# Kernel optimization log

Hardware: AMD Instinct MI355X
Metric: run time of the kernel (lower is better)

## Reference

```python
import jax, jax.numpy as jnp
import numpy as np

N, E, F_IN, F, D, L, G = 50000, 800000, 92, 128, 50, 3, 256
EPS = 1e-5


def _bn(v, g, b):
    # BatchNorm1d in training mode: biased batch stats over axis 0
    mu = jnp.mean(v, axis=0)
    var = jnp.var(v, axis=0)
    return (v - mu) * jax.lax.rsqrt(var + EPS) * g + b


def setup_inputs() -> dict:
    key = jax.random.key(0)
    ks = jax.random.split(key, 16)
    s = lambda *shape: 1.0 / np.sqrt(shape[0])
    inp = {
        "x": jax.random.normal(ks[0], (N, F_IN), dtype=jnp.float32),
        "edge_attr": jax.random.uniform(ks[1], (E, D), dtype=jnp.float32),
        # embedding MLP (2 layers, no bias)
        "w_emb0": jax.random.normal(ks[2], (F_IN, F), dtype=jnp.float32) * s(F_IN),
        "w_emb1": jax.random.normal(ks[3], (F, F), dtype=jnp.float32) * s(F),
        # CGConv params stacked over L layers; z dim = 2F + D
        "wf": jax.random.normal(ks[4], (L, 2 * F + D, F), dtype=jnp.float32) * s(2 * F + D),
        "bf": jnp.zeros((L, F), dtype=jnp.float32),
        "ws": jax.random.normal(ks[5], (L, 2 * F + D, F), dtype=jnp.float32) * s(2 * F + D),
        "bs": jnp.zeros((L, F), dtype=jnp.float32),
        "bn_g": jnp.ones((L, F), dtype=jnp.float32),
        "bn_b": jnp.zeros((L, F), dtype=jnp.float32),
        # head
        "w1": jax.random.normal(ks[6], (F, F), dtype=jnp.float32) * s(F),
        "b1": jnp.zeros((F,), dtype=jnp.float32),
        "bng": jnp.ones((F,), dtype=jnp.float32),
        "bnb": jnp.zeros((F,), dtype=jnp.float32),
        "w2": jax.random.normal(ks[7], (F, 1), dtype=jnp.float32) * s(F),
        "b2": jnp.zeros((1,), dtype=jnp.float32),
        "edge_index": jax.random.randint(ks[8], (2, E), 0, N, dtype=jnp.int64),
        "batch": jnp.sort(jax.random.randint(ks[9], (N,), 0, G, dtype=jnp.int64)),
        "num_graphs": G,
    }
    return inp


def reference(x, edge_attr, w_emb0, w_emb1, wf, bf, ws, bs, bn_g, bn_b,
              w1, b1, bng, bnb, w2, b2, edge_index, batch, num_graphs):
    src, dst = edge_index[0], edge_index[1]  # x_j = x[src], x_i = x[dst]

    # MLP embedding (bias-free), relu between layers, none after last
    h = jax.nn.relu(x @ w_emb0) @ w_emb1  # [N, F]

    gf = jnp.zeros((num_graphs, F), dtype=h.dtype)
    for l in range(L):
        z = jnp.concatenate([h[dst], h[src], edge_attr], axis=-1)  # [E, 2F+D]
        msg = jax.nn.sigmoid(z @ wf[l] + bf[l]) * jax.nn.softplus(z @ ws[l] + bs[l])
        agg = jax.ops.segment_sum(msg, dst, num_segments=N)  # scatter-add
        h = jax.nn.relu(h + _bn(agg, bn_g[l], bn_b[l]))
        gf = gf + jax.ops.segment_max(h, batch, num_segments=num_graphs)

    out = jax.nn.relu(_bn(gf @ w1 + b1, bng, bnb))
    # dropout: identity (eval mode)
    out = out @ w2 + b2  # [G, 1]
    return out.squeeze(-1)
```

## Files before the change

kernel.cpp:

```cpp
#include <hip/hip_runtime.h>
#include <hip/hip_bf16.h>

#define N_NODES 50000
#define N_EDGES 800000
#define FIN 92
#define FD 128
#define DE 50
#define NL 3
#define NG 256
#define MPAD 130
#define NW 4

typedef short short8 __attribute__((ext_vector_type(8)));
typedef float f32x4 __attribute__((ext_vector_type(4)));

__device__ __forceinline__ unsigned short f2bf(float f) {
    unsigned u = __builtin_bit_cast(unsigned, f);
    unsigned r = (u + 0x7FFFu + ((u >> 16) & 1u)) >> 16;
    return (unsigned short)r;
}
__device__ __forceinline__ float bf2f(unsigned short b) {
    unsigned u = ((unsigned)b) << 16;
    return __builtin_bit_cast(float, u);
}
__device__ __forceinline__ unsigned pack2(float a, float b) {
    return (unsigned)f2bf(a) | ((unsigned)f2bf(b) << 16);
}

__device__ __forceinline__ int posFeat(int p) {
    return ((p >> 2) & 7) * 16 + ((p >> 5) << 2) + (p & 3);
}
__device__ __forceinline__ int posFeat2(int p) {
    int q = ((p >> 5) << 3) | (p & 7);
    return ((q >> 2) << 4) + (((p >> 3) & 3) << 2) + (q & 3);
}

template<int K, int NT, int RELU, int BIAS, int OUTMODE>
__global__ __launch_bounds__(256) void gemm_bbg_kernel(
    const unsigned short* __restrict__ Abf, const unsigned short* __restrict__ Bt,
    const float* __restrict__ bias, void* __restrict__ Cout, void* __restrict__ Cout2, int M)
{
    __shared__ short Alds[64][K + 8];
    __shared__ short Blds[64][K + 8];
    const int tid = threadIdx.x;
    const int m0 = blockIdx.x * 64;
    constexpr int SEG = K / 8;
    constexpr int Nc = NT * 64;

    for (int i = tid; i < 64 * SEG; i += 256) {
        int r = i / SEG, sg = i - r * SEG;
        int row = m0 + r;
        short8 va = (row < M) ? *(const short8*)&Abf[(size_t)row * K + sg * 8] : (short8)0;
        *(short8*)&Alds[r][sg * 8] = va;
    }

    const int wv = tid >> 6, lane = tid & 63;
    const int lr = lane & 15, lk = (lane >> 4) * 8;

    for (int nt = 0; nt < NT; ++nt) {
        __syncthreads();
        for (int i = tid; i < 64 * SEG; i += 256) {
            int r = i / SEG, sg = i - r * SEG;
            *(short8*)&Blds[r][sg * 8] = *(const short8*)&Bt[(size_t)(nt * 64 + r) * K + sg * 8];
        }
        __syncthreads();

        f32x4 acc[4];
#pragma unroll
        for (int i = 0; i < 4; ++i) acc[i] = (f32x4)0.f;
#pragma unroll
        for (int k0 = 0; k0 < K; k0 += 32) {
            short8 a = *(const short8*)&Alds[wv * 16 + lr][k0 + lk];
#pragma unroll
            for (int nf = 0; nf < 4; ++nf) {
                short8 b = *(const short8*)&Blds[nf * 16 + lr][k0 + lk];
                acc[nf] = __builtin_amdgcn_mfma_f32_16x16x32_bf16(a, b, acc[nf], 0, 0, 0);
            }
        }
#pragma unroll
        for (int nf = 0; nf < 4; ++nf) {
#pragma unroll
            for (int r = 0; r < 4; ++r) {
                int row = m0 + wv * 16 + (lane >> 4) * 4 + r;
                int col = nt * 64 + nf * 16 + lr;
                if (row < M) {
                    float v = acc[nf][r];
                    if (BIAS) v += bias[col];
                    if (RELU) v = fmaxf(v, 0.f);
                    if (OUTMODE == 1) {
                        ((unsigned short*)Cout)[(size_t)row * Nc + col] = f2bf(v);
                    } else {
                        ((float*)Cout)[(size_t)row * Nc + col] = v;
                        ((unsigned short*)Cout2)[(size_t)row * Nc + col] = f2bf(v);
                    }
                }
            }
        }
    }
}

__global__ __launch_bounds__(256) void x2bf_kernel(
    const float* __restrict__ x, unsigned short* __restrict__ xbf)
{
    int i = blockIdx.x * 256 + threadIdx.x;
    if (i >= N_NODES * 96) return;
    int row = i / 96, k = i - row * 96;
    float v = (k < FIN) ? __builtin_nontemporal_load(&x[(size_t)row * FIN + k]) : 0.f;
    xbf[i] = f2bf(v);
}

__global__ __launch_bounds__(256) void build_wemb_kernel(
    const float* __restrict__ w_emb0, const float* __restrict__ w_emb1,
    unsigned short* __restrict__ w0T, unsigned short* __restrict__ w1T)
{
    int i = blockIdx.x * 256 + threadIdx.x;
    if (i < 128 * 96) {
        int n = i / 96, k = i - n * 96;
        w0T[i] = (k < FIN) ? f2bf(w_emb0[(size_t)k * FD + n]) : 0;
    }
    if (i < 128 * 128) {
        int n = i >> 7, k = i & 127;
        w1T[i] = f2bf(w_emb1[(size_t)k * FD + n]);
    }
}

__global__ __launch_bounds__(256) void build_bcatT_kernel(
    const float* __restrict__ wf, const float* __restrict__ wsw,
    const float* __restrict__ bfb, const float* __restrict__ bsb,
    unsigned short* __restrict__ BcatT, float* __restrict__ bcatF)
{
    int i = blockIdx.x * 256 + threadIdx.x;
    if (i < NL * 512 * 128) {
        int l = i / (512 * 128);
        int r = i - l * 512 * 128;
        int n = r >> 7, k = r & 127;
        int seg = n >> 7, p = n & 127;
        int nf_ = seg * 128 + posFeat2(p);
        const float* Wm = (nf_ < 256) ? wf : wsw;
        int jj = nf_ & 255;
        int krow = (jj < 128) ? k : (128 + k);
        int col = jj & 127;
        BcatT[i] = f2bf(Wm[((size_t)l * 306 + krow) * FD + col]);
    }
    if (i < NL * 512) {
        int l = i >> 9, n = i & 511;
        int seg = n >> 7, p = n & 127;
        float v = 0.f;
        if (seg == 0) v = bfb[l * FD + posFeat2(p)];
        else if (seg == 2) v = bsb[l * FD + posFeat2(p)];
        bcatF[i] = v;
    }
}

__global__ __launch_bounds__(256) void build_wecat_kernel(
    const float* __restrict__ wf, const float* __restrict__ wsw,
    unsigned short* __restrict__ WecatT)
{
    int i = blockIdx.x * 256 + threadIdx.x;
    if (i >= NL * 256 * 64) return;
    int l = i / (256 * 64);
    int r = i - l * 256 * 64;
    int col = r >> 6, k = r & 63;
    float v = 0.f;
    if (k < DE) {
        const float* W = (col < 128) ? wf : wsw;
        v = W[((size_t)l * 306 + 256 + k) * FD + (col & 127)];
    }
    WecatT[i] = f2bf(v);
}

__global__ __launch_bounds__(256) void hist_kernel(
    const int* __restrict__ dstIdx, int* __restrict__ counts)
{
    int e = blockIdx.x * 256 + threadIdx.x;
    if (e < N_EDGES) atomicAdd(&counts[dstIdx[e]], 1);
}

__global__ __launch_bounds__(1024) void scan_kernel(
    const int* __restrict__ counts, int* __restrict__ cursor)
{
    __shared__ int part[1024];
    const int t = threadIdx.x;
    const int CH = 49;
    const int base = t * CH;
    int s = 0;
    for (int i = 0; i < CH; ++i) {
        int idx = base + i;
        if (idx < N_NODES) s += counts[idx];
    }
    part[t] = s;
    __syncthreads();
    int v = s;
    for (int off = 1; off < 1024; off <<= 1) {
        int add = (t >= off) ? part[t - off] : 0;
        __syncthreads();
        v += add;
        part[t] = v;
        __syncthreads();
    }
    int pre = (t == 0) ? 0 : part[t - 1];
    for (int i = 0; i < CH; ++i) {
        int idx = base + i;
        if (idx < N_NODES) {
            cursor[idx] = pre;
            pre += counts[idx];
        }
    }
}

__global__ __launch_bounds__(256) void scatter_kernel(
    const int* __restrict__ eidx, int* __restrict__ cursor,
    int* __restrict__ perm, int* __restrict__ srcS, int* __restrict__ dstS)
{
    int e = blockIdx.x * 256 + threadIdx.x;
    if (e >= N_EDGES) return;
    int d = eidx[N_EDGES + e];
    int pos = atomicAdd(&cursor[d], 1);
    perm[pos] = e;
    srcS[pos] = eidx[e];
    dstS[pos] = d;
}

__global__ __launch_bounds__(256) void ea2bf2_kernel(
    const float* __restrict__ ea, const int* __restrict__ perm,
    unsigned* __restrict__ out)
{
    int t = blockIdx.x * 256 + threadIdx.x;
    if (t >= N_EDGES * 32) return;
    int e = t >> 5, j = t & 31;
    unsigned v = 0;
    if (j < 25) {
        int pe = perm[e];
        unsigned long long u = __builtin_nontemporal_load(
            (const unsigned long long*)(ea + (size_t)pe * DE) + j);
        float lo = __builtin_bit_cast(float, (unsigned)u);
        float hi = __builtin_bit_cast(float, (unsigned)(u >> 32));
        v = pack2(lo, hi);
    }
    out[(size_t)e * 32 + j] = v;
}

__global__ __launch_bounds__(128) void msg13_kernel(
    const unsigned short* __restrict__ Pbf,
    const unsigned short* __restrict__ eabf,
    const unsigned short* __restrict__ WecatT,
    const int* __restrict__ srcS, const int* __restrict__ dstS,
    float* __restrict__ agg)
{
    __shared__ float mlds[32][MPAD];
    __shared__ int dlds[NW * 32 + 2];
    const int tid = threadIdx.x;
    const int base = blockIdx.x * (NW * 32);

    for (int i = tid; i < NW * 32 + 2; i += 128) {
        int ge = base - 1 + i;
        int v;
        if (ge < 0) v = -1;
        else if (ge >= N_EDGES) v = -2;
        else v = __builtin_nontemporal_load(&dstS[ge]);
        dlds[i] = v;
    }

    const int w = tid >> 6, lane = tid & 63;
    const int lr = lane & 15, hi = lane >> 4;
    const int eloc = w * 16 + lr;

    int s_cur = __builtin_nontemporal_load(&srcS[base + eloc]);
    short8 b0_cur = __builtin_nontemporal_load((const short8*)&eabf[(size_t)(base + eloc) * 64 + hi * 8]);
    short8 b1_cur = __builtin_nontemporal_load((const short8*)&eabf[(size_t)(base + eloc) * 64 + 32 + hi * 8]);

    __syncthreads();

    float run = 0.f;
    bool startsInside = (dlds[1] != dlds[0]);
    const int fcol = posFeat(tid);

#pragma unroll 1
    for (int wi = 0; wi < NW; ++wi) {
        const int d = dlds[1 + wi * 32 + eloc];
        const int s = s_cur;
        const short8 b0 = b0_cur, b1 = b1_cur;

        if (wi + 1 < NW) {
            const int en = base + (wi + 1) * 32 + eloc;
            s_cur = __builtin_nontemporal_load(&srcS[en]);
            b0_cur = __builtin_nontemporal_load((const short8*)&eabf[(size_t)en * 64 + hi * 8]);
            b1_cur = __builtin_nontemporal_load((const short8*)&eabf[(size_t)en * 64 + 32 + hi * 8]);
        }

        const unsigned short* pdrow = Pbf + (size_t)d * 512 + hi * 8;
        const unsigned short* psrow = Pbf + (size_t)s * 512 + hi * 8;

        unsigned pvp[16];
        {
            short8 pds[4], pss[4];
#pragma unroll
            for (int i = 0; i < 4; ++i) {
                pds[i] = *(const short8*)(pdrow + 256 + i * 32);
                pss[i] = *(const short8*)(psrow + 384 + i * 32);
            }
            f32x4 accS[8];
#pragma unroll
            for (int i = 0; i < 8; ++i) accS[i] = (f32x4)0.f;
#pragma unroll
            for (int nf = 0; nf < 8; ++nf) {
                short8 a0 = *(const short8*)&WecatT[(size_t)((nf + 8) * 16 + lr) * 64 + hi * 8];
                short8 a1 = *(const short8*)&WecatT[(size_t)((nf + 8) * 16 + lr) * 64 + 32 + hi * 8];
                accS[nf] = __builtin_amdgcn_mfma_f32_16x16x32_bf16(a0, b0, accS[nf], 0, 0, 0);
                accS[nf] = __builtin_amdgcn_mfma_f32_16x16x32_bf16(a1, b1, accS[nf], 0, 0, 0);
            }
#pragma unroll
            for (int j = 0; j < 16; ++j) {
                const int k0 = 2 * j, k1 = 2 * j + 1;
                float v0 = accS[k0 >> 2][k0 & 3] + bf2f((unsigned short)pds[k0 >> 3][k0 & 7])
                                                 + bf2f((unsigned short)pss[k0 >> 3][k0 & 7]);
                float v1 = accS[k1 >> 2][k1 & 3] + bf2f((unsigned short)pds[k1 >> 3][k1 & 7])
                                                 + bf2f((unsigned short)pss[k1 >> 3][k1 & 7]);
                pvp[j] = pack2(v0, v1);
            }
        }

        __syncthreads();

        {
            short8 pdf[4], psf[4];
#pragma unroll
            for (int i = 0; i < 4; ++i) {
                pdf[i] = *(const short8*)(pdrow + i * 32);
                psf[i] = *(const short8*)(psrow + 128 + i * 32);
            }
            f32x4 accF[8];
#pragma unroll
            for (int i = 0; i < 8; ++i) accF[i] = (f32x4)0.f;
#pragma unroll
            for (int nf = 0; nf < 8; ++nf) {
                short8 a0 = *(const short8*)&WecatT[(size_t)(nf * 16 + lr) * 64 + hi * 8];
                short8 a1 = *(const short8*)&WecatT[(size_t)(nf * 16 + lr) * 64 + 32 + hi * 8];
                accF[nf] = __builtin_amdgcn_mfma_f32_16x16x32_bf16(a0, b0, accF[nf], 0, 0, 0);
                accF[nf] = __builtin_amdgcn_mfma_f32_16x16x32_bf16(a1, b1, accF[nf], 0, 0, 0);
            }
#pragma unroll
            for (int nf = 0; nf < 8; ++nf) {
                f32x4 m;
#pragma unroll
                for (int r = 0; r < 4; ++r) {
                    const int q = nf * 4 + r;
                    float pf = accF[nf][r] + bf2f((unsigned short)pdf[q >> 3][q & 7])
                                           + bf2f((unsigned short)psf[q >> 3][q & 7]);
                    unsigned pw = pvp[q >> 1];
                    float pv = (q & 1) ? __builtin_bit_cast(float, pw & 0xFFFF0000u)
                                       : bf2f((unsigned short)(pw & 0xFFFFu));
                    float sig = 1.f / (1.f + __expf(-pf));
                    float tt = __expf(-fabsf(pv));
                    float sp = fmaxf(pv, 0.f) + __logf(1.f + tt);
                    m[r] = sig * sp;
                }
                *(f32x4*)&mlds[eloc][hi * 32 + nf * 4] = m;
            }
        }
        __syncthreads();

        {
            const int c = tid;
#pragma unroll 4
            for (int ee = 0; ee < 32; ++ee) {
                run += mlds[ee][c];
                const int j = wi * 32 + ee;
                int de = dlds[j + 1];
                int dnext = dlds[j + 2];
                if (de != dnext) {
                    if (startsInside) agg[(size_t)de * FD + fcol] = run;
                    else unsafeAtomicAdd(&agg[(size_t)de * FD + fcol], run);
                    run = 0.f;
                    startsInside = true;
                }
            }
        }
    }
    if (run != 0.f)
        unsafeAtomicAdd(&agg[(size_t)dlds[NW * 32] * FD + fcol], run);
}

__global__ __launch_bounds__(256) void bn_stats_kernel(
    const float* __restrict__ agg, float* __restrict__ stats)
{
    __shared__ float sl[256], sql[256];
    const int tid = threadIdx.x;
    const int f = tid & 127;
    float s = 0.f, sq = 0.f;
    for (int row = blockIdx.x * 2 + (tid >> 7); row < N_NODES; row += gridDim.x * 2) {
        float v = agg[(size_t)row * FD + f];
        s += v; sq += v * v;
    }
    sl[tid] = s; sql[tid] = sq;
    __syncthreads();
    if (tid < 128) {
        unsafeAtomicAdd(&stats[f], sl[tid] + sl[tid + 128]);
        unsafeAtomicAdd(&stats[128 + f], sql[tid] + sql[tid + 128]);
    }
}

__global__ __launch_bounds__(256) void bn_update_kernel(
    float* __restrict__ h, unsigned short* __restrict__ hbf,
    const float* __restrict__ agg,
    const float* __restrict__ stats, const float* __restrict__ g,
    const float* __restrict__ b, const int* __restrict__ batch,
    float* __restrict__ gmax)
{
    const int tid = threadIdx.x;
    const int row = blockIdx.x * 2 + (tid >> 7);
    if (row >= N_NODES) return;
    const int f = tid & 127;
    const float inv = 1.f / (float)N_NODES;
    float mu = stats[f] * inv;
    float var = stats[128 + f] * inv - mu * mu;
    float rs = rsqrtf(var + 1e-5f);
    size_t idx = (size_t)row * FD + f;
    float v = h[idx] + (agg[idx] - mu) * rs * g[f] + b[f];
    v = fmaxf(v, 0.f);
    h[idx] = v;
    hbf[idx] = f2bf(v);
    atomicMax((unsigned*)&gmax[batch[row] * FD + f], __float_as_uint(v));
}

__global__ __launch_bounds__(256) void bn_gmax_kernel(
    const float* __restrict__ h, const float* __restrict__ agg,
    const float* __restrict__ stats, const float* __restrict__ g,
    const float* __restrict__ b, const int* __restrict__ batch,
    float* __restrict__ gmax)
{
    const int tid = threadIdx.x;
    const int row = blockIdx.x * 2 + (tid >> 7);
    if (row >= N_NODES) return;
    const int f = tid & 127;
    const float inv = 1.f / (float)N_NODES;
    float mu = stats[f] * inv;
    float var = stats[128 + f] * inv - mu * mu;
    float rs = rsqrtf(var + 1e-5f);
    size_t idx = (size_t)row * FD + f;
    float v = h[idx] + (agg[idx] - mu) * rs * g[f] + b[f];
    v = fmaxf(v, 0.f);
    atomicMax((unsigned*)&gmax[batch[row] * FD + f], __float_as_uint(v));
}

__global__ __launch_bounds__(256) void gf_acc_kernel(float* __restrict__ gf, const float* __restrict__ gmax)
{
    int i = blockIdx.x * 256 + threadIdx.x;
    gf[i] += gmax[i];
}

__global__ __launch_bounds__(128) void head_y_kernel(
    const float* __restrict__ gf, const float* __restrict__ w1,
    const float* __restrict__ b1, float* __restrict__ y)
{
    __shared__ float row[128];
    int g = blockIdx.x, j = threadIdx.x;
    row[j] = gf[g * FD + j];
    __syncthreads();
    float acc = b1[j];
    for (int k = 0; k < FD; ++k) acc = fmaf(row[k], w1[k * FD + j], acc);
    y[g * FD + j] = acc;
}

__global__ __launch_bounds__(128) void head_stats_kernel(
    const float* __restrict__ y, float* __restrict__ hstat)
{
    int f = threadIdx.x;
    float s = 0.f, sq = 0.f;
    for (int g = 0; g < NG; ++g) { float v = y[g * FD + f]; s += v; sq += v * v; }
    float mu = s / (float)NG;
    float var = sq / (float)NG - mu * mu;
    hstat[f] = mu;
    hstat[128 + f] = rsqrtf(var + 1e-5f);
}

__global__ __launch_bounds__(128) void head_out_kernel(
    const float* __restrict__ y, const float* __restrict__ hstat,
    const float* __restrict__ bng, const float* __restrict__ bnb,
    const float* __restrict__ w2, const float* __restrict__ b2,
    float* __restrict__ out)
{
    __shared__ float part[2];
    int g = blockIdx.x, f = threadIdx.x;
    float v = (y[g * FD + f] - hstat[f]) * hstat[128 + f] * bng[f] + bnb[f];
    v = fmaxf(v, 0.f) * w2[f];
    for (int o = 32; o > 0; o >>= 1) v += __shfl_down(v, o);
    if ((f & 63) == 0) part[f >> 6] = v;
    __syncthreads();
    if (f == 0) out[g] = part[0] + part[1] + b2[0];
}

extern "C" void kernel_launch(void* const* d_in, const int* in_sizes, int n_in,
                              void* d_out, int out_size, void* d_ws, size_t ws_size,
                              hipStream_t stream)
{
    const float* x        = (const float*)d_in[0];
    const float* edge_attr= (const float*)d_in[1];
    const float* w_emb0   = (const float*)d_in[2];
    const float* w_emb1   = (const float*)d_in[3];
    const float* wf       = (const float*)d_in[4];
    const float* bf       = (const float*)d_in[5];
    const float* wsw      = (const float*)d_in[6];
    const float* bs       = (const float*)d_in[7];
    const float* bn_g     = (const float*)d_in[8];
    const float* bn_b     = (const float*)d_in[9];
    const float* w1       = (const float*)d_in[10];
    const float* b1       = (const float*)d_in[11];
    const float* bng      = (const float*)d_in[12];
    const float* bnb      = (const float*)d_in[13];
    const float* w2       = (const float*)d_in[14];
    const float* b2       = (const float*)d_in[15];
    const int*   eidx     = (const int*)d_in[16];
    const int*   batch    = (const int*)d_in[17];

    char* base = (char*)d_ws;
    size_t off = 0;
    auto alloc = [&](size_t bytes) -> void* {
        void* p = base + off;
        off += (bytes + 255) & ~(size_t)255;
        return p;
    };
    float*          h      = (float*)alloc((size_t)N_NODES * FD * 4);
    unsigned short* hbf    = (unsigned short*)alloc((size_t)N_NODES * FD * 2);
    unsigned short* Pbf    = (unsigned short*)alloc((size_t)N_NODES * 512 * 2);
    float*          agg    = (float*)alloc((size_t)N_NODES * FD * 4);
    float*          stats  = (float*)alloc(256 * 4);
    float*          gmax   = (float*)alloc((size_t)NG * FD * 4);
    unsigned short* BcatT  = (unsigned short*)alloc((size_t)NL * 512 * 128 * 2);
    unsigned short* WecatT = (unsigned short*)alloc((size_t)NL * 256 * 64 * 2);
    float*          bcatF  = (float*)alloc((size_t)NL * 512 * 4);
    unsigned short* eabf   = (unsigned short*)alloc((size_t)N_EDGES * 64 * 2);
    int*            srcS   = (int*)alloc((size_t)N_EDGES * 4);
    int*            dstS   = (int*)alloc((size_t)N_EDGES * 4);
    unsigned short* xbf    = (unsigned short*)alloc((size_t)N_NODES * 96 * 2);
    unsigned short* w0T    = (unsigned short*)alloc((size_t)128 * 96 * 2);
    unsigned short* w1T    = (unsigned short*)alloc((size_t)128 * 128 * 2);
    float*          gf     = (float*)alloc((size_t)NG * FD * 4);
    float*          y      = (float*)alloc((size_t)NG * FD * 4);
    float*          hstat  = (float*)alloc(256 * 4);

    const size_t msetBytes = (size_t)((char*)gmax + (size_t)NG * FD * 4 - (char*)agg);

    int* perm   = (int*)agg;
    int* counts = perm + N_EDGES;
    int* cursor = counts + N_NODES;
    unsigned short* t0bf = (unsigned short*)agg;

    const int MB = (N_NODES + 63) / 64;

    hipMemsetAsync(counts, 0, (size_t)N_NODES * 4, stream);
    hist_kernel<<<(N_EDGES + 255) / 256, 256, 0, stream>>>(eidx + N_EDGES, counts);
    scan_kernel<<<1, 1024, 0, stream>>>(counts, cursor);
    scatter_kernel<<<(N_EDGES + 255) / 256, 256, 0, stream>>>(eidx, cursor, perm, srcS, dstS);
    ea2bf2_kernel<<<(N_EDGES * 32) / 256, 256, 0, stream>>>(edge_attr, perm, (unsigned*)eabf);

    build_bcatT_kernel<<<(NL * 512 * 128 + 255) / 256, 256, 0, stream>>>(wf, wsw, bf, bs, BcatT, bcatF);
    build_wecat_kernel<<<(NL * 256 * 64 + 255) / 256, 256, 0, stream>>>(wf, wsw, WecatT);
    build_wemb_kernel<<<64, 256, 0, stream>>>(w_emb0, w_emb1, w0T, w1T);
    x2bf_kernel<<<(N_NODES * 96 + 255) / 256, 256, 0, stream>>>(x, xbf);

    gemm_bbg_kernel<96, 2, 1, 0, 1><<<MB, 256, 0, stream>>>(xbf, w0T, nullptr, t0bf, nullptr, N_NODES);
    gemm_bbg_kernel<128, 2, 0, 0, 2><<<MB, 256, 0, stream>>>(t0bf, w1T, nullptr, h, hbf, N_NODES);

    hipMemsetAsync(gf, 0, (size_t)NG * FD * 4, stream);

    for (int l = 0; l < NL; ++l) {
        hipMemsetAsync(agg, 0, msetBytes, stream);

        gemm_bbg_kernel<128, 8, 0, 1, 1><<<MB, 256, 0, stream>>>(
            hbf, BcatT + (size_t)l * 512 * 128, bcatF + (size_t)l * 512, Pbf, nullptr, N_NODES);

        msg13_kernel<<<N_EDGES / (NW * 32), 128, 0, stream>>>(
            Pbf, eabf, WecatT + (size_t)l * 256 * 64, srcS, dstS, agg);

        bn_stats_kernel<<<256, 256, 0, stream>>>(agg, stats);
        if (l < NL - 1) {
            bn_update_kernel<<<(N_NODES + 1) / 2, 256, 0, stream>>>(
                h, hbf, agg, stats, bn_g + l * FD, bn_b + l * FD, batch, gmax);
        } else {
            bn_gmax_kernel<<<(N_NODES + 1) / 2, 256, 0, stream>>>(
                h, agg, stats, bn_g + l * FD, bn_b + l * FD, batch, gmax);
        }
        gf_acc_kernel<<<(NG * FD) / 256, 256, 0, stream>>>(gf, gmax);
    }

    head_y_kernel<<<NG, 128, 0, stream>>>(gf, w1, b1, y);
    head_stats_kernel<<<1, 128, 0, stream>>>(y, hstat);
    head_out_kernel<<<NG, 128, 0, stream>>>(y, hstat, bng, bnb, w2, b2, (float*)d_out);
}
```

Baseline: 1.349 ms.

## Double-buffer GEMM B tiles and msg LDS, keep A in registers, hoist gathers

The node GEMM now holds its A fragments in registers instead of LDS and double-buffers the B tiles, loading the next tile while the current one is consumed. This removes one barrier per N-tile. The message kernel double-buffers its message LDS tile, which lets it drop the barrier between the two MFMA phases, and issues all four gathered P-row loads up front to overlap gather latency. In exchange, register pressure rises in both kernels and LDS use in the message kernel doubles, which may lower occupancy.

```diff
diff --git a/kernel.cpp b/kernel.cpp
--- a/kernel.cpp
+++ b/kernel.cpp
@@ -40,41 +40,48 @@
     const unsigned short* __restrict__ Abf, const unsigned short* __restrict__ Bt,
     const float* __restrict__ bias, void* __restrict__ Cout, void* __restrict__ Cout2, int M)
 {
-    __shared__ short Alds[64][K + 8];
-    __shared__ short Blds[64][K + 8];
+    __shared__ short Blds[2][64][K + 8];
     const int tid = threadIdx.x;
     const int m0 = blockIdx.x * 64;
     constexpr int SEG = K / 8;
     constexpr int Nc = NT * 64;
+    const int wv = tid >> 6, lane = tid & 63;
+    const int lr = lane & 15, lk = (lane >> 4) * 8;
+
+    short8 afr[K / 32];
+    {
+        int arow = m0 + wv * 16 + lr;
+        bool ok = arow < M;
+#pragma unroll
+        for (int i = 0; i < K / 32; ++i)
+            afr[i] = ok ? *(const short8*)&Abf[(size_t)arow * K + i * 32 + lk] : (short8)0;
+    }
 
     for (int i = tid; i < 64 * SEG; i += 256) {
         int r = i / SEG, sg = i - r * SEG;
-        int row = m0 + r;
-        short8 va = (row < M) ? *(const short8*)&Abf[(size_t)row * K + sg * 8] : (short8)0;
-        *(short8*)&Alds[r][sg * 8] = va;
-    }
-
-    const int wv = tid >> 6, lane = tid & 63;
-    const int lr = lane & 15, lk = (lane >> 4) * 8;
+        *(short8*)&Blds[0][r][sg * 8] = *(const short8*)&Bt[(size_t)r * K + sg * 8];
+    }
+    __syncthreads();
 
     for (int nt = 0; nt < NT; ++nt) {
-        __syncthreads();
-        for (int i = tid; i < 64 * SEG; i += 256) {
-            int r = i / SEG, sg = i - r * SEG;
-            *(short8*)&Blds[r][sg * 8] = *(const short8*)&Bt[(size_t)(nt * 64 + r) * K + sg * 8];
-        }
-        __syncthreads();
+        const int cur = nt & 1;
+        if (nt + 1 < NT) {
+            for (int i = tid; i < 64 * SEG; i += 256) {
+                int r = i / SEG, sg = i - r * SEG;
+                *(short8*)&Blds[cur ^ 1][r][sg * 8] =
+                    *(const short8*)&Bt[(size_t)((nt + 1) * 64 + r) * K + sg * 8];
+            }
+        }
 
         f32x4 acc[4];
 #pragma unroll
         for (int i = 0; i < 4; ++i) acc[i] = (f32x4)0.f;
 #pragma unroll
-        for (int k0 = 0; k0 < K; k0 += 32) {
-            short8 a = *(const short8*)&Alds[wv * 16 + lr][k0 + lk];
+        for (int k0 = 0; k0 < K / 32; ++k0) {
 #pragma unroll
             for (int nf = 0; nf < 4; ++nf) {
-                short8 b = *(const short8*)&Blds[nf * 16 + lr][k0 + lk];
-                acc[nf] = __builtin_amdgcn_mfma_f32_16x16x32_bf16(a, b, acc[nf], 0, 0, 0);
+                short8 b = *(const short8*)&Blds[cur][nf * 16 + lr][k0 * 32 + lk];
+                acc[nf] = __builtin_amdgcn_mfma_f32_16x16x32_bf16(afr[k0], b, acc[nf], 0, 0, 0);
             }
         }
 #pragma unroll
@@ -96,6 +103,7 @@
                 }
             }
         }
+        __syncthreads();
     }
 }
 
@@ -240,14 +248,14 @@
     out[(size_t)e * 32 + j] = v;
 }
 
-__global__ __launch_bounds__(128) void msg13_kernel(
+__global__ __launch_bounds__(128) void msg14_kernel(
     const unsigned short* __restrict__ Pbf,
     const unsigned short* __restrict__ eabf,
     const unsigned short* __restrict__ WecatT,
     const int* __restrict__ srcS, const int* __restrict__ dstS,
     float* __restrict__ agg)
 {
-    __shared__ float mlds[32][MPAD];
+    __shared__ float mlds[2][32][MPAD];
     __shared__ int dlds[NW * 32 + 2];
     const int tid = threadIdx.x;
     const int base = blockIdx.x * (NW * 32);
@@ -280,6 +288,7 @@
         const int d = dlds[1 + wi * 32 + eloc];
         const int s = s_cur;
         const short8 b0 = b0_cur, b1 = b1_cur;
+        const int mb = wi & 1;
 
         if (wi + 1 < NW) {
             const int en = base + (wi + 1) * 32 + eloc;
@@ -291,14 +300,17 @@
         const unsigned short* pdrow = Pbf + (size_t)d * 512 + hi * 8;
         const unsigned short* psrow = Pbf + (size_t)s * 512 + hi * 8;
 
+        short8 pds[4], pss[4], pdf[4], psf[4];
+#pragma unroll
+        for (int i = 0; i < 4; ++i) {
+            pds[i] = *(const short8*)(pdrow + 256 + i * 32);
+            pss[i] = *(const short8*)(psrow + 384 + i * 32);
+            pdf[i] = *(const short8*)(pdrow + i * 32);
+            psf[i] = *(const short8*)(psrow + 128 + i * 32);
+        }
+
         unsigned pvp[16];
         {
-            short8 pds[4], pss[4];
-#pragma unroll
-            for (int i = 0; i < 4; ++i) {
-                pds[i] = *(const short8*)(pdrow + 256 + i * 32);
-                pss[i] = *(const short8*)(psrow + 384 + i * 32);
-            }
             f32x4 accS[8];
 #pragma unroll
             for (int i = 0; i < 8; ++i) accS[i] = (f32x4)0.f;
@@ -320,15 +332,7 @@
             }
         }
 
-        __syncthreads();
-
         {
-            short8 pdf[4], psf[4];
-#pragma unroll
-            for (int i = 0; i < 4; ++i) {
-                pdf[i] = *(const short8*)(pdrow + i * 32);
-                psf[i] = *(const short8*)(psrow + 128 + i * 32);
-            }
             f32x4 accF[8];
 #pragma unroll
             for (int i = 0; i < 8; ++i) accF[i] = (f32x4)0.f;
@@ -355,7 +359,7 @@
                     float sp = fmaxf(pv, 0.f) + __logf(1.f + tt);
                     m[r] = sig * sp;
                 }
-                *(f32x4*)&mlds[eloc][hi * 32 + nf * 4] = m;
+                *(f32x4*)&mlds[mb][eloc][hi * 32 + nf * 4] = m;
             }
         }
         __syncthreads();
@@ -364,7 +368,7 @@
             const int c = tid;
 #pragma unroll 4
             for (int ee = 0; ee < 32; ++ee) {
-                run += mlds[ee][c];
+                run += mlds[mb][ee][c];
                 const int j = wi * 32 + ee;
                 int de = dlds[j + 1];
                 int dnext = dlds[j + 2];
@@ -570,7 +574,7 @@
         gemm_bbg_kernel<128, 8, 0, 1, 1><<<MB, 256, 0, stream>>>(
             hbf, BcatT + (size_t)l * 512 * 128, bcatF + (size_t)l * 512, Pbf, nullptr, N_NODES);
 
-        msg13_kernel<<<N_EDGES / (NW * 32), 128, 0, stream>>>(
+        msg14_kernel<<<N_EDGES / (NW * 32), 128, 0, stream>>>(
             Pbf, eabf, WecatT + (size_t)l * 256 * 64, srcS, dstS, agg);
 
         bn_stats_kernel<<<256, 256, 0, stream>>>(agg, stats);
```

Measured after the change: 1.649 ms. 22.2% more time.

## Give each wave its own edge span and drop block-wide barriers in message kernel

Applied to the files above, without the earlier changes.

The message kernel now gives each wave a contiguous 64-edge span. It processes 16 edges per iteration and keeps a private LDS tile per wave. Each lane holds two running sums covering all 128 feature columns for the segmented scatter reduction. This removes the two block-wide __syncthreads per iteration, so waves can progress independently. In exchange there are more segment boundaries handled with atomics at wave edges, and each lane does twice the reduction work per edge.

```diff
diff --git a/kernel.cpp b/kernel.cpp
--- a/kernel.cpp
+++ b/kernel.cpp
@@ -240,14 +240,14 @@
     out[(size_t)e * 32 + j] = v;
 }
 
-__global__ __launch_bounds__(128) void msg13_kernel(
+__global__ __launch_bounds__(128) void msg15_kernel(
     const unsigned short* __restrict__ Pbf,
     const unsigned short* __restrict__ eabf,
     const unsigned short* __restrict__ WecatT,
     const int* __restrict__ srcS, const int* __restrict__ dstS,
     float* __restrict__ agg)
 {
-    __shared__ float mlds[32][MPAD];
+    __shared__ float mlds[2][16][MPAD];
     __shared__ int dlds[NW * 32 + 2];
     const int tid = threadIdx.x;
     const int base = blockIdx.x * (NW * 32);
@@ -263,26 +263,30 @@
 
     const int w = tid >> 6, lane = tid & 63;
     const int lr = lane & 15, hi = lane >> 4;
-    const int eloc = w * 16 + lr;
-
-    int s_cur = __builtin_nontemporal_load(&srcS[base + eloc]);
-    short8 b0_cur = __builtin_nontemporal_load((const short8*)&eabf[(size_t)(base + eloc) * 64 + hi * 8]);
-    short8 b1_cur = __builtin_nontemporal_load((const short8*)&eabf[(size_t)(base + eloc) * 64 + 32 + hi * 8]);
+    const int wspan = w * 64;
+
+    {
+    }
+    int s_cur = __builtin_nontemporal_load(&srcS[base + wspan + lr]);
+    short8 b0_cur = __builtin_nontemporal_load((const short8*)&eabf[(size_t)(base + wspan + lr) * 64 + hi * 8]);
+    short8 b1_cur = __builtin_nontemporal_load((const short8*)&eabf[(size_t)(base + wspan + lr) * 64 + 32 + hi * 8]);
 
     __syncthreads();
 
-    float run = 0.f;
-    bool startsInside = (dlds[1] != dlds[0]);
-    const int fcol = posFeat(tid);
+    float run0 = 0.f, run1 = 0.f;
+    bool startsInside = (dlds[wspan + 1] != dlds[wspan]);
+    const int fc0 = posFeat(lane);
+    const int fc1 = posFeat(lane + 64);
 
 #pragma unroll 1
     for (int wi = 0; wi < NW; ++wi) {
-        const int d = dlds[1 + wi * 32 + eloc];
+        const int jbase = wspan + wi * 16;
+        const int d = dlds[1 + jbase + lr];
         const int s = s_cur;
         const short8 b0 = b0_cur, b1 = b1_cur;
 
         if (wi + 1 < NW) {
-            const int en = base + (wi + 1) * 32 + eloc;
+            const int en = base + jbase + 16 + lr;
             s_cur = __builtin_nontemporal_load(&srcS[en]);
             b0_cur = __builtin_nontemporal_load((const short8*)&eabf[(size_t)en * 64 + hi * 8]);
             b1_cur = __builtin_nontemporal_load((const short8*)&eabf[(size_t)en * 64 + 32 + hi * 8]);
@@ -319,8 +323,6 @@
                 pvp[j] = pack2(v0, v1);
             }
         }
-
-        __syncthreads();
 
         {
             short8 pdf[4], psf[4];
@@ -355,30 +357,36 @@
                     float sp = fmaxf(pv, 0.f) + __logf(1.f + tt);
                     m[r] = sig * sp;
                 }
-                *(f32x4*)&mlds[eloc][hi * 32 + nf * 4] = m;
-            }
-        }
-        __syncthreads();
+                *(f32x4*)&mlds[w][lr][hi * 32 + nf * 4] = m;
+            }
+        }
 
         {
-            const int c = tid;
 #pragma unroll 4
-            for (int ee = 0; ee < 32; ++ee) {
-                run += mlds[ee][c];
-                const int j = wi * 32 + ee;
+            for (int ee = 0; ee < 16; ++ee) {
+                const int j = jbase + ee;
+                run0 += mlds[w][ee][lane];
+                run1 += mlds[w][ee][lane + 64];
                 int de = dlds[j + 1];
                 int dnext = dlds[j + 2];
                 if (de != dnext) {
-                    if (startsInside) agg[(size_t)de * FD + fcol] = run;
-                    else unsafeAtomicAdd(&agg[(size_t)de * FD + fcol], run);
-                    run = 0.f;
+                    if (startsInside) {
+                        agg[(size_t)de * FD + fc0] = run0;
+                        agg[(size_t)de * FD + fc1] = run1;
+                    } else {
+                        unsafeAtomicAdd(&agg[(size_t)de * FD + fc0], run0);
+                        unsafeAtomicAdd(&agg[(size_t)de * FD + fc1], run1);
+                    }
+                    run0 = 0.f; run1 = 0.f;
                     startsInside = true;
                 }
             }
         }
     }
-    if (run != 0.f)
-        unsafeAtomicAdd(&agg[(size_t)dlds[NW * 32] * FD + fcol], run);
+    if (run0 != 0.f || run1 != 0.f) {
+        unsafeAtomicAdd(&agg[(size_t)dlds[wspan + 64] * FD + fc0], run0);
+        unsafeAtomicAdd(&agg[(size_t)dlds[wspan + 64] * FD + fc1], run1);
+    }
 }
 
 __global__ __launch_bounds__(256) void bn_stats_kernel(
@@ -570,7 +578,7 @@
         gemm_bbg_kernel<128, 8, 0, 1, 1><<<MB, 256, 0, stream>>>(
             hbf, BcatT + (size_t)l * 512 * 128, bcatF + (size_t)l * 512, Pbf, nullptr, N_NODES);
 
-        msg13_kernel<<<N_EDGES / (NW * 32), 128, 0, stream>>>(
+        msg15_kernel<<<N_EDGES / (NW * 32), 128, 0, stream>>>(
             Pbf, eabf, WecatT + (size_t)l * 256 * 64, srcS, dstS, agg);
 
         bn_stats_kernel<<<256, 256, 0, stream>>>(agg, stats);
```

After: 1.279 ms. 1.05x faster.
